# Kernel optimization log

Measured on AMD Instinct MI355X. Metric: run time of the kernel, lower is better.

The kernel has to match this reference:

```python
import jax, jax.numpy as jnp
import numpy as np

B, IN_C, OUT_C, K, Z_DIM = 32, 128, 128, 3, 512
H, W, STRIDE = 56, 56, 1


def setup_inputs() -> dict:
    key = jax.random.key(0)
    k1, k2, k3 = jax.random.split(key, 3)
    x = jax.random.normal(k1, (B, IN_C, H, W), dtype=jnp.float32)
    z = jax.random.normal(k2, (B, Z_DIM), dtype=jnp.float32)
    # nn.Linear(z_dim, out_c*in_c*k*k): weight [out_f, in_f], bias [out_f]
    out_f = OUT_C * IN_C * K * K
    W_head = jax.random.normal(k3, (out_f, Z_DIM), dtype=jnp.float32) * (1.0 / np.sqrt(Z_DIM))
    b_head = jnp.zeros((out_f,), dtype=jnp.float32)
    return {"x": x, "z": z, "W_head": W_head, "b_head": b_head}


def reference(x, z, W_head, b_head):
    b = x.shape[0]
    # hypernetwork head: per-sample conv weights
    w = z @ W_head.T + b_head                       # [B, out_c*in_c*k*k]
    w = w.reshape(b, OUT_C, IN_C, K, K)             # [B, O, I, K, K]

    pad = K // 2

    def conv_one(xi, wi):
        # xi: [I, H, W], wi: [O, I, K, K] -> [O, H', W']
        out = jax.lax.conv_general_dilated(
            xi[None],                                # [1, I, H, W]
            wi,
            window_strides=(STRIDE, STRIDE),
            padding=[(pad, pad), (pad, pad)],
            dimension_numbers=("NCHW", "OIHW", "NCHW"),
        )
        return out[0]

    return jax.vmap(conv_one)(x, w)                 # [B, O, H', W']
```

## Files before the change

kernel.cpp:

```cpp
#include <hip/hip_runtime.h>
#include <hip/hip_bf16.h>
#include <stdint.h>

#define BB 32
#define IC 128
#define OC 128
#define HH 56
#define WW 56
#define ZD 512
#define NRS 9
#define OI (OC*IC)
#define WROWS (OI*NRS)
#define WDIM 58
#define NHEADBLK 1024
#define NTRBLK (HH * BB)
#define XTILE (4 * WDIM * 256)

typedef float  f32x4  __attribute__((ext_vector_type(4)));
typedef short  bf16x8 __attribute__((ext_vector_type(8)));
typedef short  s16x4  __attribute__((ext_vector_type(4)));

static __device__ __forceinline__ short f2bf(float f) {
    uint32_t u = __float_as_uint(f);
    uint32_t r = (u + 0x7fffu + ((u >> 16) & 1u)) >> 16;
    return (short)r;
}
static __device__ __forceinline__ short f2bf_hw(float f) {
    __hip_bfloat16 h = __float2bfloat16(f);
    return *reinterpret_cast<short*>(&h);
}
static __device__ __forceinline__ float bf2f(short s) {
    uint32_t u = ((uint32_t)(uint16_t)s) << 16;
    return __uint_as_float(u);
}
static __device__ __forceinline__ void gll16(const void* g, void* l) {
    __builtin_amdgcn_global_load_lds(
        (const __attribute__((address_space(1))) uint32_t*)g,
        (__attribute__((address_space(3))) uint32_t*)l, 16, 0, 0);
}

__global__ __launch_bounds__(576, 1) void fused_head_tr_kernel(
    const float* __restrict__ Wh, const float* __restrict__ z,
    const float* __restrict__ bh, short* __restrict__ wbf,
    const float* __restrict__ x, short* __restrict__ xt)
{
    if (blockIdx.x >= NHEADBLK) {
        const int bx = blockIdx.x - NHEADBLK;
        const int b = bx / HH;
        const int h = bx - b * HH;
        const int tid = threadIdx.x;
        if (tid >= 512) return;
        const int w = tid & 63;
        const int yq = tid >> 6;
        if (w >= WW) return;
        const float* xp = x + (size_t)b * IC * HH * WW + h * WW + w;
        short* op = xt + (((size_t)(b * HH + h)) * WW + w) * IC;
        #pragma unroll
        for (int q = 0; q < 2; ++q) {
            int ic = yq * 2 + q;
            bf16x8 pk;
            #pragma unroll
            for (int j = 0; j < 8; ++j) {
                float v = xp[(size_t)(ic * 8 + j) * (HH * WW)];
                pk[j] = f2bf(v);
            }
            *(bf16x8*)(op + ic * 8) = pk;
        }
        return;
    }

    __shared__ __align__(16) char Zl[32 * 1024];
    __shared__ __align__(16) char Sl[144 * 64];
    const int tid  = threadIdx.x;
    const int lane = tid & 63;
    const int wv   = tid >> 6;

    if (tid < 256) {
        const int b = tid >> 3, ks = (tid & 7) * 64;
        const float* zp = z + (size_t)b * ZD + ks;
        const int bx = (b & 7) << 4;
        #pragma unroll
        for (int j8 = 0; j8 < 8; ++j8) {
            f32x4 v0 = *(const f32x4*)(zp + j8 * 8);
            f32x4 v1 = *(const f32x4*)(zp + j8 * 8 + 4);
            bf16x8 pk;
            pk[0] = f2bf_hw(v0.x); pk[1] = f2bf_hw(v0.y);
            pk[2] = f2bf_hw(v0.z); pk[3] = f2bf_hw(v0.w);
            pk[4] = f2bf_hw(v1.x); pk[5] = f2bf_hw(v1.y);
            pk[6] = f2bf_hw(v1.z); pk[7] = f2bf_hw(v1.w);
            *(bf16x8*)(Zl + b * 1024 + ((ks * 2 + j8 * 16) ^ bx)) = pk;
        }
    }
    __syncthreads();

    const int rl = lane & 15;
    const int kq = lane >> 4;
    const int zxor = (rl & 7) << 4;
    const int rowLocal = wv * 16 + rl;
    const int rowg = blockIdx.x * 144 + rowLocal;

    const char* wp = (const char*)Wh + (size_t)rowg * (ZD * 4) + kq * 32;

    f32x4 wd[16];
    #pragma unroll
    for (int i = 0; i < 8; ++i) {
        wd[2 * i]     = *(const f32x4*)(wp + i * 128);
        wd[2 * i + 1] = *(const f32x4*)(wp + i * 128 + 16);
    }

    f32x4 acc0 = {0.f, 0.f, 0.f, 0.f}, acc1 = {0.f, 0.f, 0.f, 0.f};
    #pragma unroll
    for (int kb = 0; kb < 16; ++kb) {
        const int sl = kb & 7;
        const int koff = (kb * 64 + kq * 16) ^ zxor;
        bf16x8 a0 = *(const bf16x8*)(Zl + rl * 1024 + koff);
        bf16x8 a1 = *(const bf16x8*)(Zl + (16 + rl) * 1024 + koff);
        f32x4 lo = wd[2 * sl];
        f32x4 hi = wd[2 * sl + 1];
        bf16x8 bw;
        bw[0] = f2bf_hw(lo.x); bw[1] = f2bf_hw(lo.y);
        bw[2] = f2bf_hw(lo.z); bw[3] = f2bf_hw(lo.w);
        bw[4] = f2bf_hw(hi.x); bw[5] = f2bf_hw(hi.y);
        bw[6] = f2bf_hw(hi.z); bw[7] = f2bf_hw(hi.w);
        acc0 = __builtin_amdgcn_mfma_f32_16x16x32_bf16(a0, bw, acc0, 0, 0, 0);
        acc1 = __builtin_amdgcn_mfma_f32_16x16x32_bf16(a1, bw, acc1, 0, 0, 0);
        if (kb < 8) {
            wd[2 * sl]     = *(const f32x4*)(wp + (kb + 8) * 128);
            wd[2 * sl + 1] = *(const f32x4*)(wp + (kb + 8) * 128 + 16);
        }
    }

    {
        const int swz = (rowLocal & 7) << 3;
        s16x4 s0, s1;
        #pragma unroll
        for (int reg = 0; reg < 4; ++reg) {
            s0[reg] = f2bf(acc0[reg]);
            s1[reg] = f2bf(acc1[reg]);
        }
        *(s16x4*)(Sl + rowLocal * 64 + ((kq * 8) ^ swz))      = s0;
        *(s16x4*)(Sl + rowLocal * 64 + ((32 + kq * 8) ^ swz)) = s1;
    }
    __syncthreads();

    if (tid < 512) {
        const int b  = tid >> 4;
        const int oiL = tid & 15;
        const int oi = blockIdx.x * 16 + oiL;
        #pragma unroll
        for (int rs = 0; rs < 9; ++rs) {
            const int rowL = oiL * 9 + rs;
            short sh = *(const short*)(Sl + rowL * 64 +
                                       ((2 * b) ^ ((rowL & 7) << 3)));
            float v = bf2f(sh) + bh[(size_t)oi * 9 + rs];
            wbf[((size_t)(b * 9 + rs)) * OI + oi] = f2bf(v);
        }
    }
}

__global__ __launch_bounds__(256) void conv_kernel(
    const short* __restrict__ wbf,
    const short* __restrict__ xt,
    float* __restrict__ out)
{
    __shared__ __align__(16) char Xl[XTILE];
    __shared__ __align__(16) char Wl[3][32768];
    const int tid  = threadIdx.x;
    const int lane = tid & 63;
    const int wv   = tid >> 6;
    const int og   = wv & 1;
    const int hh   = wv >> 1;
    const int h0 = blockIdx.x * 2;
    const int b  = blockIdx.y;

    #pragma unroll
    for (int q = 0; q < 15; ++q) {
        int idx = tid + q * 256;
        if (idx < XTILE / 16) ((f32x4*)Xl)[idx] = (f32x4){0.f, 0.f, 0.f, 0.f};
    }
    __syncthreads();

    for (int r = 0; r < 4; ++r) {
        int hin = h0 + r - 1;
        if (hin < 0 || hin >= HH) continue;
        const char* src = (const char*)(xt + ((size_t)(b * HH + hin)) * WW * IC);
        char* dstb = Xl + (r * WDIM + 1) * 256;
        for (int it = wv; it < 14; it += 4) {
            int c = it * 64 + lane;
            int u = r * WDIM + 1 + (c >> 4);
            int soff = (c * 16) ^ ((u & 7) << 4);
            gll16(src + soff, dstb + it * 1024);
        }
    }

    #define STAGE_CW(rs_, buf_)                                                 \
        {                                                                       \
            const char* ws_ = (const char*)(wbf +                               \
                ((size_t)b * NRS + (rs_)) * OI);                                \
            _Pragma("unroll")                                                   \
            for (int it_ = 0; it_ < 8; ++it_) {                                 \
                int c_ = (wv * 8 + it_) * 64 + lane;                            \
                int so_ = (c_ * 16) ^ (((c_ >> 4) & 7) << 4);                   \
                gll16(ws_ + so_, Wl[buf_] + (wv * 8 + it_) * 1024);             \
            }                                                                   \
        }

    STAGE_CW(0, 0);

    f32x4 acc[4][4];
    #pragma unroll
    for (int a = 0; a < 4; ++a)
        #pragma unroll
        for (int p = 0; p < 4; ++p) acc[a][p] = (f32x4){0.f, 0.f, 0.f, 0.f};

    const int axor = (lane & 7) << 4;
    int kkoff[4];
    #pragma unroll
    for (int kk = 0; kk < 4; ++kk) kkoff[kk] = kk * 64 + ((lane >> 4) << 4);

    for (int rs = 0; rs < 9; ++rs) {
        if (rs < 8) STAGE_CW(rs + 1, (rs + 1) % 3);
        if (rs == 8) { asm volatile("s_waitcnt vmcnt(0)" ::: "memory"); }
        else         { asm volatile("s_waitcnt vmcnt(8)" ::: "memory"); }
        __builtin_amdgcn_sched_barrier(0);
        __builtin_amdgcn_s_barrier();
        __builtin_amdgcn_sched_barrier(0);

        const char* Wb = Wl[rs % 3];
        const int r = rs / 3, s = rs - 3 * r;
        int ubase[4], bswz[4];
        #pragma unroll
        for (int pf = 0; pf < 4; ++pf) {
            int p = pf * 16 + (lane & 15);
            int pc = p > 55 ? 55 : p;
            int uu = (hh + r) * WDIM + pc + s;
            ubase[pf] = uu * 256;
            bswz[pf] = (uu & 7) << 4;
        }
        #pragma unroll
        for (int kk = 0; kk < 4; ++kk) {
            bf16x8 av[4];
            #pragma unroll
            for (int af = 0; af < 4; ++af)
                av[af] = *(const bf16x8*)(Wb + (og * 64 + af * 16 + (lane & 15)) * 256 +
                                          (kkoff[kk] ^ axor));
            #pragma unroll
            for (int pf = 0; pf < 4; ++pf) {
                bf16x8 bv = *(const bf16x8*)(Xl + ubase[pf] + (kkoff[kk] ^ bswz[pf]));
                #pragma unroll
                for (int af = 0; af < 4; ++af)
                    acc[af][pf] = __builtin_amdgcn_mfma_f32_16x16x32_bf16(
                        av[af], bv, acc[af][pf], 0, 0, 0);
            }
        }
    }
    #undef STAGE_CW

    const int pcol = lane & 15;
    const int rowq = lane >> 4;
    const int hO = h0 + hh;
    #pragma unroll
    for (int af = 0; af < 4; ++af) {
        int o0 = og * 64 + af * 16 + rowq * 4;
        #pragma unroll
        for (int pf = 0; pf < 4; ++pf) {
            int p = pf * 16 + pcol;
            if (p < WW) {
                #pragma unroll
                for (int reg = 0; reg < 4; ++reg) {
                    out[(((size_t)b * OC + (o0 + reg)) * HH + hO) * WW + p] = acc[af][pf][reg];
                }
            }
        }
    }
}

extern "C" void kernel_launch(void* const* d_in, const int* in_sizes, int n_in,
                              void* d_out, int out_size, void* d_ws, size_t ws_size,
                              hipStream_t stream) {
    const float* x  = (const float*)d_in[0];
    const float* z  = (const float*)d_in[1];
    const float* Wh = (const float*)d_in[2];
    const float* bh = (const float*)d_in[3];
    float* out = (float*)d_out;

    short* wbf = (short*)d_ws;
    short* xt  = (short*)((char*)d_ws + 9437184);

    fused_head_tr_kernel<<<dim3(NHEADBLK + NTRBLK), 576, 0, stream>>>(Wh, z, bh, wbf, x, xt);
    conv_kernel<<<dim3(HH / 2, BB), 256, 0, stream>>>(wbf, xt, out);
}
```

Measured before the change: 153.8 us.

## Read padded input directly from global memory and register-stage conv weights

The transpose kernel now writes a zero-padded NHWC bf16 input (58x58) with its borders zeroed. This lets the conv kernel skip the LDS input tile and read B-fragments straight from global/L2 memory. Weight staging changes from async global_load_lds triple buffering to register prefetch plus LDS double buffering with two block barriers per step. Blocks are remapped onto a 1D grid with an XCD-aware swizzle so that blocks sharing a batch sit on the same XCD. The change saves LDS and the input staging cost, but it adds global-latency loads of activations inside the MFMA loop.

```diff
diff --git a/kernel.cpp b/kernel.cpp
--- a/kernel.cpp
+++ b/kernel.cpp
@@ -11,10 +11,11 @@
 #define NRS 9
 #define OI (OC*IC)
 #define WROWS (OI*NRS)
-#define WDIM 58
 #define NHEADBLK 1024
 #define NTRBLK (HH * BB)
-#define XTILE (4 * WDIM * 256)
+#define XP 58
+#define XROW (XP * IC)
+#define XBAT ((size_t)XP * XP * IC)
 
 typedef float  f32x4  __attribute__((ext_vector_type(4)));
 typedef short  bf16x8 __attribute__((ext_vector_type(8)));
@@ -33,38 +34,48 @@
     uint32_t u = ((uint32_t)(uint16_t)s) << 16;
     return __uint_as_float(u);
 }
-static __device__ __forceinline__ void gll16(const void* g, void* l) {
-    __builtin_amdgcn_global_load_lds(
-        (const __attribute__((address_space(1))) uint32_t*)g,
-        (__attribute__((address_space(3))) uint32_t*)l, 16, 0, 0);
-}
 
 __global__ __launch_bounds__(576, 1) void fused_head_tr_kernel(
     const float* __restrict__ Wh, const float* __restrict__ z,
     const float* __restrict__ bh, short* __restrict__ wbf,
-    const float* __restrict__ x, short* __restrict__ xt)
+    const float* __restrict__ x, short* __restrict__ xtp)
 {
     if (blockIdx.x >= NHEADBLK) {
         const int bx = blockIdx.x - NHEADBLK;
         const int b = bx / HH;
         const int h = bx - b * HH;
         const int tid = threadIdx.x;
-        if (tid >= 512) return;
-        const int w = tid & 63;
-        const int yq = tid >> 6;
-        if (w >= WW) return;
-        const float* xp = x + (size_t)b * IC * HH * WW + h * WW + w;
-        short* op = xt + (((size_t)(b * HH + h)) * WW + w) * IC;
-        #pragma unroll
-        for (int q = 0; q < 2; ++q) {
-            int ic = yq * 2 + q;
-            bf16x8 pk;
-            #pragma unroll
-            for (int j = 0; j < 8; ++j) {
-                float v = xp[(size_t)(ic * 8 + j) * (HH * WW)];
-                pk[j] = f2bf(v);
+        short* xb = xtp + (size_t)b * XBAT;
+
+        if (tid < 512) {
+            const int w = tid & 63;
+            const int yq = tid >> 6;
+            if (w < WW) {
+                const float* xp = x + (size_t)b * IC * HH * WW + h * WW + w;
+                short* op = xb + ((size_t)(h + 1) * XP + (w + 1)) * IC;
+                #pragma unroll
+                for (int q = 0; q < 2; ++q) {
+                    int ic = yq * 2 + q;
+                    bf16x8 pk;
+                    #pragma unroll
+                    for (int j = 0; j < 8; ++j) {
+                        float v = xp[(size_t)(ic * 8 + j) * (HH * WW)];
+                        pk[j] = f2bf(v);
+                    }
+                    *(bf16x8*)(op + ic * 8) = pk;
+                }
             }
-            *(bf16x8*)(op + ic * 8) = pk;
+        } else if (tid < 544) {
+            int t = tid - 512;
+            int u = (t >> 4) * (XP - 1);
+            *(f32x4*)((char*)(xb + ((size_t)(h + 1) * XP + u) * IC) + (t & 15) * 16) =
+                (f32x4){0.f, 0.f, 0.f, 0.f};
+        }
+        if (h == 0 || h == HH - 1) {
+            const int v = (h == 0) ? 0 : XP - 1;
+            char* rowp = (char*)(xb + (size_t)v * XROW);
+            for (int idx = tid; idx < XROW * 2 / 16; idx += 576)
+                *(f32x4*)(rowp + idx * 16) = (f32x4){0.f, 0.f, 0.f, 0.f};
         }
         return;
     }
@@ -160,52 +171,45 @@
 
 __global__ __launch_bounds__(256) void conv_kernel(
     const short* __restrict__ wbf,
-    const short* __restrict__ xt,
+    const short* __restrict__ xtp,
     float* __restrict__ out)
 {
-    __shared__ __align__(16) char Xl[XTILE];
-    __shared__ __align__(16) char Wl[3][32768];
+    __shared__ __align__(16) char Wl[2][32768];
     const int tid  = threadIdx.x;
     const int lane = tid & 63;
     const int wv   = tid >> 6;
     const int og   = wv & 1;
     const int hh   = wv >> 1;
-    const int h0 = blockIdx.x * 2;
-    const int b  = blockIdx.y;
-
-    #pragma unroll
-    for (int q = 0; q < 15; ++q) {
-        int idx = tid + q * 256;
-        if (idx < XTILE / 16) ((f32x4*)Xl)[idx] = (f32x4){0.f, 0.f, 0.f, 0.f};
-    }
-    __syncthreads();
-
-    for (int r = 0; r < 4; ++r) {
-        int hin = h0 + r - 1;
-        if (hin < 0 || hin >= HH) continue;
-        const char* src = (const char*)(xt + ((size_t)(b * HH + hin)) * WW * IC);
-        char* dstb = Xl + (r * WDIM + 1) * 256;
-        for (int it = wv; it < 14; it += 4) {
-            int c = it * 64 + lane;
-            int u = r * WDIM + 1 + (c >> 4);
-            int soff = (c * 16) ^ ((u & 7) << 4);
-            gll16(src + soff, dstb + it * 1024);
-        }
-    }
-
-    #define STAGE_CW(rs_, buf_)                                                 \
+
+    const int bid = blockIdx.x;
+    const int wg  = (bid & 7) * 112 + (bid >> 3);
+    const int b   = wg / 28;
+    const int h0  = (wg - b * 28) * 2;
+
+    const short* xb = xtp + (size_t)b * XBAT;
+    const int rl = lane & 15;
+    const int kq = lane >> 4;
+
+    f32x4 wr[8];
+    #define WLOAD(rs_)                                                          \
         {                                                                       \
-            const char* ws_ = (const char*)(wbf +                               \
-                ((size_t)b * NRS + (rs_)) * OI);                                \
+            const char* ws_ = (const char*)(wbf + ((size_t)b * NRS + (rs_)) * OI); \
             _Pragma("unroll")                                                   \
             for (int it_ = 0; it_ < 8; ++it_) {                                 \
                 int c_ = (wv * 8 + it_) * 64 + lane;                            \
                 int so_ = (c_ * 16) ^ (((c_ >> 4) & 7) << 4);                   \
-                gll16(ws_ + so_, Wl[buf_] + (wv * 8 + it_) * 1024);             \
+                wr[it_] = *(const f32x4*)(ws_ + so_);                           \
             }                                                                   \
         }
-
-    STAGE_CW(0, 0);
+    #define WSTORE(buf_)                                                        \
+        _Pragma("unroll")                                                       \
+        for (int it_ = 0; it_ < 8; ++it_)                                       \
+            *(f32x4*)(Wl[buf_] + (wv * 8 + it_) * 1024 + lane * 16) = wr[it_];
+
+    WLOAD(0);
+    WSTORE(0);
+    __syncthreads();
+    WLOAD(1);
 
     f32x4 acc[4][4];
     #pragma unroll
@@ -216,55 +220,50 @@
     const int axor = (lane & 7) << 4;
     int kkoff[4];
     #pragma unroll
-    for (int kk = 0; kk < 4; ++kk) kkoff[kk] = kk * 64 + ((lane >> 4) << 4);
+    for (int kk = 0; kk < 4; ++kk) kkoff[kk] = kk * 64 + (kq << 4);
 
     for (int rs = 0; rs < 9; ++rs) {
-        if (rs < 8) STAGE_CW(rs + 1, (rs + 1) % 3);
-        if (rs == 8) { asm volatile("s_waitcnt vmcnt(0)" ::: "memory"); }
-        else         { asm volatile("s_waitcnt vmcnt(8)" ::: "memory"); }
-        __builtin_amdgcn_sched_barrier(0);
-        __builtin_amdgcn_s_barrier();
-        __builtin_amdgcn_sched_barrier(0);
-
-        const char* Wb = Wl[rs % 3];
         const int r = rs / 3, s = rs - 3 * r;
-        int ubase[4], bswz[4];
+        const char* Wb = Wl[rs & 1];
+        const short* xrow = xb + (size_t)(h0 + hh + r) * XROW;
+        int uoff[4];
         #pragma unroll
         for (int pf = 0; pf < 4; ++pf) {
-            int p = pf * 16 + (lane & 15);
+            int p = pf * 16 + rl;
             int pc = p > 55 ? 55 : p;
-            int uu = (hh + r) * WDIM + pc + s;
-            ubase[pf] = uu * 256;
-            bswz[pf] = (uu & 7) << 4;
+            uoff[pf] = (pc + s) * IC + kq * 8;
         }
         #pragma unroll
         for (int kk = 0; kk < 4; ++kk) {
             bf16x8 av[4];
             #pragma unroll
             for (int af = 0; af < 4; ++af)
-                av[af] = *(const bf16x8*)(Wb + (og * 64 + af * 16 + (lane & 15)) * 256 +
+                av[af] = *(const bf16x8*)(Wb + (og * 64 + af * 16 + rl) * 256 +
                                           (kkoff[kk] ^ axor));
             #pragma unroll
             for (int pf = 0; pf < 4; ++pf) {
-                bf16x8 bv = *(const bf16x8*)(Xl + ubase[pf] + (kkoff[kk] ^ bswz[pf]));
+                bf16x8 bv = *(const bf16x8*)(xrow + uoff[pf] + kk * 32);
                 #pragma unroll
                 for (int af = 0; af < 4; ++af)
                     acc[af][pf] = __builtin_amdgcn_mfma_f32_16x16x32_bf16(
                         av[af], bv, acc[af][pf], 0, 0, 0);
             }
         }
-    }
-    #undef STAGE_CW
-
-    const int pcol = lane & 15;
-    const int rowq = lane >> 4;
+        __syncthreads();
+        if (rs < 8) { WSTORE((rs & 1) ^ 1); }
+        if (rs < 7) { WLOAD(rs + 2); }
+        __syncthreads();
+    }
+    #undef WLOAD
+    #undef WSTORE
+
     const int hO = h0 + hh;
     #pragma unroll
     for (int af = 0; af < 4; ++af) {
-        int o0 = og * 64 + af * 16 + rowq * 4;
+        int o0 = og * 64 + af * 16 + kq * 4;
         #pragma unroll
         for (int pf = 0; pf < 4; ++pf) {
-            int p = pf * 16 + pcol;
+            int p = pf * 16 + rl;
             if (p < WW) {
                 #pragma unroll
                 for (int reg = 0; reg < 4; ++reg) {
@@ -285,8 +284,8 @@
     float* out = (float*)d_out;
 
     short* wbf = (short*)d_ws;
-    short* xt  = (short*)((char*)d_ws + 9437184);
-
-    fused_head_tr_kernel<<<dim3(NHEADBLK + NTRBLK), 576, 0, stream>>>(Wh, z, bh, wbf, x, xt);
-    conv_kernel<<<dim3(HH / 2, BB), 256, 0, stream>>>(wbf, xt, out);
-}
+    short* xtp = (short*)((char*)d_ws + 9437184);
+
+    fused_head_tr_kernel<<<dim3(NHEADBLK + NTRBLK), 576, 0, stream>>>(Wh, z, bh, wbf, x, xtp);
+    conv_kernel<<<dim3(28 * 32), 256, 0, stream>>>(wbf, xtp, out);
+}
```

New measurement: 167.5 us. 8.9% more time.
